# Optimization experiments

Measured on AMD Instinct MI355X. Metric: run time of the kernel, lower is better.

## Reference

```python
import jax, jax.numpy as jnp
import numpy as np
from jax import lax

T = 32
TAU = 2.0
ALPHA = 2.0
V_TH = 1.0
V_RESET = 0.0
MAX_ACTION = 1.0
HID = 750

# ATan surrogate spike function (spikingjelly surrogate.ATan with alpha=2.0)
@jax.custom_vjp
def atan_spike(x):
    return (x >= 0.0).astype(x.dtype)

def _spike_fwd(x):
    return atan_spike(x), x

def _spike_bwd(x, g):
    # d/dx [1/pi * atan(pi/2 * alpha * x) + 1/2] = (alpha/2) / (1 + (pi/2*alpha*x)^2)
    return (g * (ALPHA / 2.0) / (1.0 + (jnp.pi / 2.0 * ALPHA * x) ** 2),)

atan_spike.defvjp(_spike_fwd, _spike_bwd)


def lif_seq(x_seq):
    """MultiStepLIFNode with decay_input=True, hard reset. x_seq: [T,B,D] -> spikes [T,B,D]."""
    def step(v, x):
        h = v + (x - (v - V_RESET)) / TAU  # neuronal_charge
        s = atan_spike(h - V_TH)           # neuronal_fire
        v_new = h * (1.0 - s) + V_RESET * s  # hard reset
        return v_new, s
    v0 = jnp.zeros_like(x_seq[0])
    _, spikes = lax.scan(step, v0, x_seq)
    return spikes


def seq_linear(x_seq, W, b):
    # x_seq: [T,B,I], W: [O,I], b: [O]
    return jnp.einsum('tbi,oi->tbo', x_seq, W) + b


def nonspiking_out(x_seq):
    # NonSpikingLIFNode.forward receives the whole [T,B,D] seq (override bypasses the step loop):
    # v starts at 0 scalar -> v = 0 + (x - (0 - v_reset))/tau = x/tau (v_reset=0), shape [T,B,D]
    return (x_seq + V_RESET) / TAU - 0.0 + 0.0 if False else x_seq / TAU


def setup_inputs() -> dict:
    key = jax.random.key(0)
    ks = jax.random.split(key, 20)
    B, SD, AD, LD = 2048, 256, 64, 128
    def lin(kw, kb, o, i):
        bound = 1.0 / np.sqrt(i)
        W = jax.random.uniform(kw, (o, i), jnp.float32, -bound, bound)
        b = jax.random.uniform(kb, (o,), jnp.float32, -bound, bound)
        return W, b
    W1, b1 = lin(ks[0], ks[1], HID, SD + AD)
    W2, b2 = lin(ks[2], ks[3], HID, HID)
    Wm, bm = lin(ks[4], ks[5], LD, HID)
    Wls, bls = lin(ks[6], ks[7], LD, HID)
    Wd1, bd1 = lin(ks[8], ks[9], HID, SD + LD)
    Wd2, bd2 = lin(ks[10], ks[11], HID, HID)
    Wd3, bd3 = lin(ks[12], ks[13], AD, HID)
    return {
        'state': jax.random.normal(ks[14], (B, SD), jnp.float32),
        'action': jax.random.normal(ks[15], (B, AD), jnp.float32),
        'eps': jax.random.normal(ks[16], (B, LD), jnp.float32),
        'W1': W1, 'b1': b1, 'W2': W2, 'b2': b2,
        'Wm': Wm, 'bm': bm, 'Wls': Wls, 'bls': bls,
        'Wd1': Wd1, 'bd1': bd1, 'Wd2': Wd2, 'bd2': bd2, 'Wd3': Wd3, 'bd3': bd3,
    }


def reference(state, action, eps, W1, b1, W2, b2, Wm, bm, Wls, bls, Wd1, bd1, Wd2, bd2, Wd3, bd3):
    B = state.shape[0]
    # Encoder
    x = jnp.concatenate([state, action], axis=1)            # [B, SD+AD]
    x_seq = jnp.broadcast_to(x, (T,) + x.shape)             # repeat(T,1,1)
    z = lif_seq(seq_linear(x_seq, W1, b1))                  # e1
    z = lif_seq(seq_linear(z, W2, b2))                      # e2
    mean = jnp.max(seq_linear(z, Wm, bm) / TAU, axis=0)     # NonSpiking v = x/tau, then max over T
    log_std = jnp.max(seq_linear(z, Wls, bls) / TAU, axis=0)
    log_std = jnp.clip(log_std, -4.0, 15.0)
    std = jnp.exp(log_std)
    zlat = mean + std * eps
    # Decoder
    d_in = jnp.concatenate([state, zlat], axis=1)
    d_seq = jnp.broadcast_to(d_in, (T,) + d_in.shape)
    a = lif_seq(seq_linear(d_seq, Wd1, bd1))
    a = lif_seq(seq_linear(a, Wd2, bd2))
    a = jnp.max(seq_linear(a, Wd3, bd3) / TAU, axis=0)
    u = MAX_ACTION * jnp.tanh(a)
    return (u, mean, std)
```

## Files before the change

### kernel.cpp

```cpp
#include <hip/hip_runtime.h>
#include <math.h>

#define TT   32
#define NB   2048
#define SDIM 256
#define ADIM 64
#define LDIM 128
#define HID  750
#define KP   768
#define KW   24
#define EIN  320
#define DIN  384
#define NSTEP 12

typedef float    f32x4 __attribute__((ext_vector_type(4)));
typedef int      i32x4 __attribute__((ext_vector_type(4)));
typedef unsigned u32x4 __attribute__((ext_vector_type(4)));

__device__ __forceinline__ f32x4 mfma16(u32x4 a, u32x4 b, f32x4 c) {
    asm("v_mfma_f32_16x16x32_bf16 %0, %1, %2, %0" : "+v"(c) : "v"(a), "v"(b));
    return c;
}
__device__ __forceinline__ i32x4 mfma_i8(u32x4 a, u32x4 b, i32x4 c) {
    asm("v_mfma_i32_16x16x64_i8 %0, %1, %2, %0" : "+v"(c) : "v"(a), "v"(b));
    return c;
}

__device__ __forceinline__ void gload_lds16(void* lds, const void* g) {
    __builtin_amdgcn_global_load_lds(
        (const __attribute__((address_space(1))) unsigned int*)g,
        (__attribute__((address_space(3))) unsigned int*)lds, 16, 0, 0);
}

__device__ __forceinline__ void bfsplit(float v, unsigned& hb, unsigned& lb) {
    unsigned u = __float_as_uint(v);
    hb = (u + 0x7FFFu + ((u >> 16) & 1u)) >> 16;
    float res = v - __uint_as_float(hb << 16);
    unsigned u2 = __float_as_uint(res);
    lb = (u2 + 0x7FFFu + ((u2 >> 16) & 1u)) >> 16;
}

#define I8_E1 589824
#define I8_E2 1179648
#define I8_E3 1277952
#define I8_E4 1376256
#define I8_E5 1425408
__global__ void wsplit_i8_all(const float* __restrict__ W2,
                              const float* __restrict__ Wd2,
                              const float* __restrict__ Wm,
                              const float* __restrict__ Wls,
                              const float* __restrict__ Wd3,
                              char* __restrict__ W2h,  char* __restrict__ W2l,
                              char* __restrict__ Wd2h, char* __restrict__ Wd2l,
                              char* __restrict__ WmlsH, char* __restrict__ WmlsL,
                              char* __restrict__ Wu3h, char* __restrict__ Wu3l) {
    int i = blockIdx.x * blockDim.x + threadIdx.x;
    if (i >= I8_E5) return;
    const float* src; char* dh; char* dl; int rvalid, o_base;
    if (i < I8_E1)      { src = W2;  dh = W2h;  dl = W2l;  rvalid = HID;  o_base = 0; }
    else if (i < I8_E2) { i -= I8_E1; src = Wd2; dh = Wd2h; dl = Wd2l; rvalid = HID;  o_base = 0; }
    else if (i < I8_E3) { i -= I8_E2; src = Wm;  dh = WmlsH; dl = WmlsL; rvalid = LDIM; o_base = 0; }
    else if (i < I8_E4) { i -= I8_E3; src = Wls; dh = WmlsH; dl = WmlsL; rvalid = LDIM; o_base = 128; }
    else                { i -= I8_E4; src = Wd3; dh = Wu3h; dl = Wu3l; rvalid = ADIM; o_base = 0; }
    int r = i / KP, k = i % KP;
    float v = (r < rvalid && k < HID) ? src[r * HID + k] : 0.f;
    int q = (int)rintf(v * 524288.f);
    int lo = (q << 24) >> 24;
    int hi = (q - lo) >> 8;
    int o = o_base + r;
    size_t di = (size_t)((o >> 6) * NSTEP + (k >> 6)) * 4096
              + ((k >> 4) & 3) * 1024 + (o & 63) * 16 + (k & 15);
    dh[di] = (char)hi;
    dl[di] = (char)lo;
}

#define BF_E1 245760
#define BF_E2 540672
__global__ void wsplit_bf_all(const float* __restrict__ W1,
                              const float* __restrict__ Wd1,
                              unsigned short* __restrict__ W1h,
                              unsigned short* __restrict__ W1l,
                              unsigned short* __restrict__ Wd1h,
                              unsigned short* __restrict__ Wd1l) {
    int i = blockIdx.x * blockDim.x + threadIdx.x;
    if (i >= BF_E2) return;
    const float* src; unsigned short* dh; unsigned short* dl; int K, KS;
    if (i < BF_E1) { src = W1; dh = W1h; dl = W1l; K = EIN; KS = 5; }
    else { i -= BF_E1; src = Wd1; dh = Wd1h; dl = Wd1l; K = DIN; KS = 6; }
    int r = i / K, k = i % K;
    float v = (r < HID) ? src[r * K + k] : 0.f;
    unsigned hb, lb;
    bfsplit(v, hb, lb);
    size_t di = ((size_t)((r >> 6) * KS + (k >> 6)) * 8
               + ((k >> 5) & 1) * 4 + ((k >> 3) & 3)) * 512 + (r & 63) * 8 + (k & 7);
    dh[di] = (unsigned short)hb;
    dl[di] = (unsigned short)lb;
}

__global__ void concat_xsplit_enc(const float* __restrict__ state,
                                  const float* __restrict__ action,
                                  unsigned short* __restrict__ Xh,
                                  unsigned short* __restrict__ Xl) {
    int t = blockIdx.x * blockDim.x + threadIdx.x;
    if (t >= NB * (EIN / 8)) return;
    int b = t & (NB - 1), c8 = t >> 11;
    float vals[8];
    if (c8 < SDIM / 8) {
        const float* src = state + (size_t)b * SDIM + c8 * 8;
#pragma unroll
        for (int j = 0; j < 8; ++j) vals[j] = src[j];
    } else {
        const float* src = action + (size_t)b * ADIM + (c8 * 8 - SDIM);
#pragma unroll
        for (int j = 0; j < 8; ++j) vals[j] = src[j];
    }
    unsigned hs[8], ls[8];
#pragma unroll
    for (int j = 0; j < 8; ++j) bfsplit(vals[j], hs[j], ls[j]);
    u32x4 ph, pl;
#pragma unroll
    for (int j = 0; j < 4; ++j) {
        ph[j] = hs[2 * j] | (hs[2 * j + 1] << 16);
        pl[j] = ls[2 * j] | (ls[2 * j + 1] << 16);
    }
    *(u32x4*)(Xh + (size_t)t * 8) = ph;
    *(u32x4*)(Xl + (size_t)t * 8) = pl;
}

__global__ void latent_xsplit(const float* __restrict__ mean_ws,
                              const float* __restrict__ ls_ws,
                              const float* __restrict__ eps,
                              const float* __restrict__ state,
                              float* __restrict__ out,
                              unsigned short* __restrict__ Xh,
                              unsigned short* __restrict__ Xl) {
    int t = blockIdx.x * blockDim.x + threadIdx.x;
    if (t >= NB * (DIN / 8)) return;
    int b = t & (NB - 1), c8 = t >> 11;
    float vals[8];
    if (c8 < SDIM / 8) {
        const float* src = state + (size_t)b * SDIM + c8 * 8;
#pragma unroll
        for (int j = 0; j < 8; ++j) vals[j] = src[j];
    } else {
        int o0 = c8 * 8 - SDIM;
#pragma unroll
        for (int j = 0; j < 8; ++j) {
            int o = o0 + j;
            float m = mean_ws[(size_t)b * LDIM + o];
            float l = ls_ws[(size_t)b * LDIM + o];
            l = fminf(fmaxf(l, -4.0f), 15.0f);
            float s = expf(l);
            vals[j] = m + s * eps[(size_t)b * LDIM + o];
            out[NB * ADIM + (size_t)b * LDIM + o] = m;
            out[NB * ADIM + NB * LDIM + (size_t)b * LDIM + o] = s;
        }
    }
    unsigned hs[8], ls[8];
#pragma unroll
    for (int j = 0; j < 8; ++j) bfsplit(vals[j], hs[j], ls[j]);
    u32x4 ph, pl;
#pragma unroll
    for (int j = 0; j < 4; ++j) {
        ph[j] = hs[2 * j] | (hs[2 * j + 1] << 16);
        pl[j] = ls[2 * j] | (ls[2 * j + 1] << 16);
    }
    *(u32x4*)(Xh + (size_t)t * 8) = ph;
    *(u32x4*)(Xl + (size_t)t * 8) = pl;
}

template<int KS>
__global__ __launch_bounds__(256)
void lif1(const unsigned short* __restrict__ Ah,
          const unsigned short* __restrict__ Al,
          const unsigned short* __restrict__ Wh,
          const unsigned short* __restrict__ Wl,
          const float* __restrict__ bias,
          unsigned* __restrict__ obitsT) {
    __shared__ __align__(16) char smraw[32768];
    const int tid = threadIdx.x, wave = tid >> 6, l = tid & 63;
    const int kg = l >> 4, li = l & 15;
    const int nb = blockIdx.x, n0 = nb * 64, mb = blockIdx.y;
    const int r0 = mb * 128 + wave * 32;
    f32x4 acc[2][4] = {};

    auto stage = [&](int buf, int step) {
        const char* sH = (const char*)(Wh + (size_t)(nb * KS + step) * 4096);
        const char* sL = (const char*)(Wl + (size_t)(nb * KS + step) * 4096);
        char* d = smraw + buf * 16384;
#pragma unroll
        for (int j = 0; j < 2; ++j) {
            gload_lds16(d + j * 4096 + tid * 16, sH + j * 4096 + tid * 16);
            gload_lds16(d + 8192 + j * 4096 + tid * 16, sL + j * 4096 + tid * 16);
        }
    };

    stage(0, 0);
    for (int step = 0; step < KS; ++step) {
        asm volatile("s_waitcnt vmcnt(0)" ::: "memory");
        __builtin_amdgcn_s_barrier();
        __builtin_amdgcn_sched_barrier(0);
        u32x4 ah[2][2], al2[2][2];
#pragma unroll
        for (int kc = 0; kc < 2; ++kc)
#pragma unroll
            for (int mt = 0; mt < 2; ++mt) {
                int r = r0 + mt * 16 + li;
                size_t aoff = ((size_t)(step * 8 + kc * 4 + kg) * NB + r) * 8;
                ah[kc][mt]  = *(const u32x4*)(Ah + aoff);
                al2[kc][mt] = *(const u32x4*)(Al + aoff);
            }
        if (step + 1 < KS) stage((step + 1) & 1, step + 1);
        const char* bufB = smraw + (step & 1) * 16384;
        __builtin_amdgcn_s_setprio(1);
#pragma unroll
        for (int kc = 0; kc < 2; ++kc) {
#pragma unroll
            for (int nt = 0; nt < 4; ++nt) {
                int boff = (kc * 4 + kg) * 1024 + (nt * 16 + li) * 16;
                u32x4 bh = *(const u32x4*)(bufB + boff);
                u32x4 bl = *(const u32x4*)(bufB + 8192 + boff);
#pragma unroll
                for (int mt = 0; mt < 2; ++mt) {
                    acc[mt][nt] = mfma16(ah[kc][mt], bh, acc[mt][nt]);
                    acc[mt][nt] = mfma16(ah[kc][mt], bl, acc[mt][nt]);
                    acc[mt][nt] = mfma16(al2[kc][mt], bh, acc[mt][nt]);
                }
            }
        }
        __builtin_amdgcn_s_setprio(0);
    }
    __syncthreads();

    unsigned* Sb = (unsigned*)smraw;
#pragma unroll
    for (int nt = 0; nt < 4; ++nt) {
        int o = n0 + nt * 16 + li;
        float bo = (o < HID) ? bias[o] : 0.f;
#pragma unroll
        for (int mt = 0; mt < 2; ++mt)
#pragma unroll
            for (int r = 0; r < 4; ++r) {
                float c = acc[mt][nt][r] + bo;
                float v = 0.f;
                unsigned sb = 0u;
#pragma unroll
                for (int t = 0; t < TT; ++t) {
                    float h = 0.5f * (v + c);
                    if (h >= 1.0f) { sb |= (1u << t); v = 0.f; }
                    else           { v = h; }
                }
                Sb[(wave * 32 + mt * 16 + kg * 4 + r) * 64 + nt * 16 + li] = sb;
            }
    }
    __syncthreads();

    for (int rr = 0; rr < 32; ++rr) {
        int row = wave * 32 + rr;
        unsigned wv = Sb[row * 64 + l];
        unsigned myw = 0;
#pragma unroll
        for (int t = 0; t < TT; ++t) {
            unsigned long long m = __ballot((wv >> t) & 1u);
            if ((l & 31) == t) myw = (l < 32) ? (unsigned)m : (unsigned)(m >> 32);
        }
        int b = mb * 128 + row;
        obitsT[((size_t)b * KW + nb * 2 + (l >= 32)) * TT + (l & 31)] = myw;
    }
}

template<int EPI>
__global__ __launch_bounds__(256)
void bitgemm(const unsigned* __restrict__ bitsT,
             const char* __restrict__ Wh,
             const char* __restrict__ Wl,
             const float* __restrict__ bias,
             const float* __restrict__ bias2,
             unsigned* __restrict__ obitsT,
             float* __restrict__ o0,
             float* __restrict__ o1) {
    __shared__ __align__(16) char smraw[32768];
    const int tid = threadIdx.x;
    const int w = tid >> 6, l = tid & 63;
    const int kg = l >> 4, li = l & 15;
    const int nb = blockIdx.x, n0 = nb * 64;
    const int by = blockIdx.y;
    const int b = by * 4 + w;
    const unsigned fld = (kg & 1) * 16;

    i32x4 acc[2][4][2] = {};

    auto stage = [&](int s) {
        char* d = smraw + (s & 3) * 8192;
        const char* sH = Wh + (size_t)(nb * NSTEP + s) * 4096;
        const char* sL = Wl + (size_t)(nb * NSTEP + s) * 4096;
        gload_lds16(d + tid * 16, sH + tid * 16);
        gload_lds16(d + 4096 + tid * 16, sL + tid * 16);
    };
    auto loadA = [&](int s, unsigned (&aw)[2]) {
#pragma unroll
        for (int mt = 0; mt < 2; ++mt)
            aw[mt] = bitsT[((size_t)b * KW + s * 2 + (kg >> 1)) * TT + mt * 16 + li];
    };
    auto compute = [&](int s, const unsigned (&aw)[2]) {
        const char* bufB = smraw + (s & 3) * 8192;
        u32x4 afrag[2];
#pragma unroll
        for (int mt = 0; mt < 2; ++mt) {
            unsigned wv = aw[mt] >> fld;
            u32x4 a;
#pragma unroll
            for (int j = 0; j < 4; ++j)
                a[j] = __umul24((wv >> (4 * j)) & 0xFu, 0x00204081u) & 0x01010101u;
            afrag[mt] = a;
        }
        __builtin_amdgcn_s_setprio(1);
#pragma unroll
        for (int nt = 0; nt < 4; ++nt) {
            int boff = kg * 1024 + (nt * 16 + li) * 16;
            u32x4 bh = *(const u32x4*)(bufB + boff);
            u32x4 bl = *(const u32x4*)(bufB + 4096 + boff);
#pragma unroll
            for (int mt = 0; mt < 2; ++mt) {
                acc[mt][nt][0] = mfma_i8(afrag[mt], bh, acc[mt][nt][0]);
                acc[mt][nt][1] = mfma_i8(afrag[mt], bl, acc[mt][nt][1]);
            }
        }
        __builtin_amdgcn_s_setprio(0);
    };

    unsigned aw[2], awn[2];
    stage(0);
    asm volatile("s_waitcnt vmcnt(0)" ::: "memory");
    __builtin_amdgcn_s_barrier();
    stage(1);
    loadA(0, aw);

    for (int s = 0; s < NSTEP; ++s) {
        asm volatile("s_waitcnt vmcnt(4)" ::: "memory");
        __builtin_amdgcn_s_barrier();
        __builtin_amdgcn_sched_barrier(0);
        if (s + 2 < NSTEP) stage(s + 2);
        if (s + 1 < NSTEP) loadA(s + 1, awn);
        compute(s, aw);
        aw[0] = awn[0];
        aw[1] = awn[1];
    }
    __syncthreads();

    float* Sf = (float*)smraw;
#pragma unroll
    for (int p = 0; p < 2; ++p) {
#pragma unroll
        for (int mt = 0; mt < 2; ++mt)
#pragma unroll
            for (int ntl = 0; ntl < 2; ++ntl) {
                int nt = p * 2 + ntl;
#pragma unroll
                for (int r = 0; r < 4; ++r) {
                    int cmb = (acc[mt][nt][0][r] << 8) + acc[mt][nt][1][r];
                    Sf[(w * 32 + mt * 16 + kg * 4 + r) * 34 + ntl * 16 + li]
                        = (float)cmb * (1.f / 524288.f);
                }
            }
        __syncthreads();

        if (l < 32) {
            int c = l;
            int o = n0 + p * 32 + c;
            if (EPI == 0) {
                float bo = (o < HID) ? bias[o] : 0.f;
                float v = 0.f;
                unsigned sb = 0u;
#pragma unroll
                for (int t = 0; t < TT; ++t) {
                    float h = 0.5f * (v + Sf[(w * 32 + t) * 34 + c] + bo);
                    if (h >= 1.0f) { sb |= (1u << t); v = 0.f; }
                    else           { v = h; }
                }
                if (o >= HID) sb = 0u;
                unsigned myw = 0;
#pragma unroll
                for (int t = 0; t < TT; ++t) {
                    unsigned long long m = __ballot((sb >> t) & 1u);
                    if (l == t) myw = (unsigned)m;
                }
                obitsT[((size_t)b * KW + nb * 2 + p) * TT + l] = myw;
            } else {
                float mx = -1e30f;
#pragma unroll
                for (int t = 0; t < TT; ++t)
                    mx = fmaxf(mx, Sf[(w * 32 + t) * 34 + c]);
                if (EPI == 1) {
                    float bo = (o < LDIM) ? bias[o] : bias2[o - LDIM];
                    float val = 0.5f * (mx + bo);
                    if (o < LDIM) o0[(size_t)b * LDIM + o] = val;
                    else          o1[(size_t)b * LDIM + (o - LDIM)] = val;
                } else {
                    o0[(size_t)b * ADIM + o] = tanhf(0.5f * (mx + bias[o]));
                }
            }
        }
        __syncthreads();
    }
}

extern "C" void kernel_launch(void* const* d_in, const int* in_sizes, int n_in,
                              void* d_out, int out_size, void* d_ws, size_t ws_size,
                              hipStream_t stream) {
    const float* state  = (const float*)d_in[0];
    const float* action = (const float*)d_in[1];
    const float* eps    = (const float*)d_in[2];
    const float* W1  = (const float*)d_in[3];
    const float* b1  = (const float*)d_in[4];
    const float* W2  = (const float*)d_in[5];
    const float* b2  = (const float*)d_in[6];
    const float* Wm  = (const float*)d_in[7];
    const float* bm  = (const float*)d_in[8];
    const float* Wls = (const float*)d_in[9];
    const float* bls = (const float*)d_in[10];
    const float* Wd1 = (const float*)d_in[11];
    const float* bd1 = (const float*)d_in[12];
    const float* Wd2 = (const float*)d_in[13];
    const float* bd2 = (const float*)d_in[14];
    const float* Wd3 = (const float*)d_in[15];
    const float* bd3 = (const float*)d_in[16];
    float* out = (float*)d_out;

    char* ws = (char*)d_ws;
    size_t off = 0;
    auto alloc = [&](size_t bytes) {
        void* p = ws + off;
        off += (bytes + 255) & ~(size_t)255;
        return p;
    };
    unsigned*       bitsT_a = (unsigned*)alloc((size_t)NB * TT * KW * 4);
    unsigned*       bitsT_b = (unsigned*)alloc((size_t)NB * TT * KW * 4);
    float*          mean_ws = (float*)   alloc((size_t)NB * LDIM * 4);
    float*          ls_ws   = (float*)   alloc((size_t)NB * LDIM * 4);
    unsigned short* Xh      = (unsigned short*)alloc((size_t)NB * DIN * 2);
    unsigned short* Xl      = (unsigned short*)alloc((size_t)NB * DIN * 2);
    char*           W2h     = (char*)alloc((size_t)KP * KP);
    char*           W2l     = (char*)alloc((size_t)KP * KP);
    char*           Wd2h    = (char*)alloc((size_t)KP * KP);
    char*           Wd2l    = (char*)alloc((size_t)KP * KP);
    char*           WmlsH   = (char*)alloc((size_t)256 * KP);
    char*           WmlsL   = (char*)alloc((size_t)256 * KP);
    char*           Wu3h    = (char*)alloc((size_t)64 * KP);
    char*           Wu3l    = (char*)alloc((size_t)64 * KP);
    unsigned short* W1h     = (unsigned short*)alloc((size_t)KP * EIN * 2);
    unsigned short* W1l     = (unsigned short*)alloc((size_t)KP * EIN * 2);
    unsigned short* Wd1h    = (unsigned short*)alloc((size_t)KP * DIN * 2);
    unsigned short* Wd1l    = (unsigned short*)alloc((size_t)KP * DIN * 2);

    dim3 blk(256);

    wsplit_i8_all<<<(I8_E5 + 255) / 256, blk, 0, stream>>>(
        W2, Wd2, Wm, Wls, Wd3, W2h, W2l, Wd2h, Wd2l, WmlsH, WmlsL, Wu3h, Wu3l);
    wsplit_bf_all<<<(BF_E2 + 255) / 256, blk, 0, stream>>>(
        W1, Wd1, W1h, W1l, Wd1h, Wd1l);

    concat_xsplit_enc<<<(NB * (EIN / 8) + 255) / 256, blk, 0, stream>>>(state, action, Xh, Xl);
    lif1<5><<<dim3(12, 16), blk, 0, stream>>>(Xh, Xl, W1h, W1l, b1, bitsT_a);
    bitgemm<0><<<dim3(12, NB / 4), blk, 0, stream>>>(bitsT_a, W2h, W2l, b2, nullptr,
                                                     bitsT_b, nullptr, nullptr);
    bitgemm<1><<<dim3(4, NB / 4), blk, 0, stream>>>(bitsT_b, WmlsH, WmlsL, bm, bls,
                                                    nullptr, mean_ws, ls_ws);
    latent_xsplit<<<(NB * (DIN / 8) + 255) / 256, blk, 0, stream>>>(
        mean_ws, ls_ws, eps, state, out, Xh, Xl);

    lif1<6><<<dim3(12, 16), blk, 0, stream>>>(Xh, Xl, Wd1h, Wd1l, bd1, bitsT_a);
    bitgemm<0><<<dim3(12, NB / 4), blk, 0, stream>>>(bitsT_a, Wd2h, Wd2l, bd2, nullptr,
                                                     bitsT_b, nullptr, nullptr);
    bitgemm<2><<<dim3(1, NB / 4), blk, 0, stream>>>(bitsT_b, Wu3h, Wu3l, bd3, nullptr,
                                                    nullptr, out, nullptr);
}
```

Before: 269.1 us.

## Halve lif1 row tile for more blocks; per-wave bitgemm epilogue without block barriers

lif1 now gives each wave 16 rows instead of 32, so each block covers 64 rows and the grid doubles to 12x32 blocks. The intent is better occupancy and a smaller register footprint, at the cost of reloading the staged weight tiles twice as often. The bitgemm epilogue now gives each wave its own padded shared-memory region and processes all 64 columns in one pass with all lanes active. This removes the two-phase loop and the block-wide barriers inside it, and drops the barrier between the LIF and transpose stages in lif1, since those stages now only touch wave-private shared memory. Shared memory in bitgemm grows slightly to fit the per-wave staging.

```diff
diff --git a/kernel.cpp b/kernel.cpp
--- a/kernel.cpp
+++ b/kernel.cpp
@@ -178,11 +178,11 @@
           const float* __restrict__ bias,
           unsigned* __restrict__ obitsT) {
     __shared__ __align__(16) char smraw[32768];
-    const int tid = threadIdx.x, wave = tid >> 6, l = tid & 63;
+    const int tid = threadIdx.x, w = tid >> 6, l = tid & 63;
     const int kg = l >> 4, li = l & 15;
     const int nb = blockIdx.x, n0 = nb * 64, mb = blockIdx.y;
-    const int r0 = mb * 128 + wave * 32;
-    f32x4 acc[2][4] = {};
+    const int r0 = mb * 64 + w * 16;
+    f32x4 acc[4] = {};
 
     auto stage = [&](int buf, int step) {
         const char* sH = (const char*)(Wh + (size_t)(nb * KS + step) * 4096);
@@ -200,16 +200,13 @@
         asm volatile("s_waitcnt vmcnt(0)" ::: "memory");
         __builtin_amdgcn_s_barrier();
         __builtin_amdgcn_sched_barrier(0);
-        u32x4 ah[2][2], al2[2][2];
-#pragma unroll
-        for (int kc = 0; kc < 2; ++kc)
-#pragma unroll
-            for (int mt = 0; mt < 2; ++mt) {
-                int r = r0 + mt * 16 + li;
-                size_t aoff = ((size_t)(step * 8 + kc * 4 + kg) * NB + r) * 8;
-                ah[kc][mt]  = *(const u32x4*)(Ah + aoff);
-                al2[kc][mt] = *(const u32x4*)(Al + aoff);
-            }
+        u32x4 ah[2], al2[2];
+#pragma unroll
+        for (int kc = 0; kc < 2; ++kc) {
+            size_t aoff = ((size_t)(step * 8 + kc * 4 + kg) * NB + r0 + li) * 8;
+            ah[kc]  = *(const u32x4*)(Ah + aoff);
+            al2[kc] = *(const u32x4*)(Al + aoff);
+        }
         if (step + 1 < KS) stage((step + 1) & 1, step + 1);
         const char* bufB = smraw + (step & 1) * 16384;
         __builtin_amdgcn_s_setprio(1);
@@ -220,12 +217,9 @@
                 int boff = (kc * 4 + kg) * 1024 + (nt * 16 + li) * 16;
                 u32x4 bh = *(const u32x4*)(bufB + boff);
                 u32x4 bl = *(const u32x4*)(bufB + 8192 + boff);
-#pragma unroll
-                for (int mt = 0; mt < 2; ++mt) {
-                    acc[mt][nt] = mfma16(ah[kc][mt], bh, acc[mt][nt]);
-                    acc[mt][nt] = mfma16(ah[kc][mt], bl, acc[mt][nt]);
-                    acc[mt][nt] = mfma16(al2[kc][mt], bh, acc[mt][nt]);
-                }
+                acc[nt] = mfma16(ah[kc], bh, acc[nt]);
+                acc[nt] = mfma16(ah[kc], bl, acc[nt]);
+                acc[nt] = mfma16(al2[kc], bh, acc[nt]);
             }
         }
         __builtin_amdgcn_s_setprio(0);
@@ -238,25 +232,22 @@
         int o = n0 + nt * 16 + li;
         float bo = (o < HID) ? bias[o] : 0.f;
 #pragma unroll
-        for (int mt = 0; mt < 2; ++mt)
-#pragma unroll
-            for (int r = 0; r < 4; ++r) {
-                float c = acc[mt][nt][r] + bo;
-                float v = 0.f;
-                unsigned sb = 0u;
-#pragma unroll
-                for (int t = 0; t < TT; ++t) {
-                    float h = 0.5f * (v + c);
-                    if (h >= 1.0f) { sb |= (1u << t); v = 0.f; }
-                    else           { v = h; }
-                }
-                Sb[(wave * 32 + mt * 16 + kg * 4 + r) * 64 + nt * 16 + li] = sb;
+        for (int r = 0; r < 4; ++r) {
+            float c = acc[nt][r] + bo;
+            float v = 0.f;
+            unsigned sb = 0u;
+#pragma unroll
+            for (int t = 0; t < TT; ++t) {
+                float h = 0.5f * (v + c);
+                if (h >= 1.0f) { sb |= (1u << t); v = 0.f; }
+                else           { v = h; }
             }
-    }
-    __syncthreads();
-
-    for (int rr = 0; rr < 32; ++rr) {
-        int row = wave * 32 + rr;
+            Sb[(w * 16 + kg * 4 + r) * 64 + nt * 16 + li] = sb;
+        }
+    }
+
+    for (int rr = 0; rr < 16; ++rr) {
+        int row = w * 16 + rr;
         unsigned wv = Sb[row * 64 + l];
         unsigned myw = 0;
 #pragma unroll
@@ -264,7 +255,7 @@
             unsigned long long m = __ballot((wv >> t) & 1u);
             if ((l & 31) == t) myw = (l < 32) ? (unsigned)m : (unsigned)(m >> 32);
         }
-        int b = mb * 128 + row;
+        int b = mb * 64 + row;
         obitsT[((size_t)b * KW + nb * 2 + (l >= 32)) * TT + (l & 31)] = myw;
     }
 }
@@ -279,7 +270,7 @@
              unsigned* __restrict__ obitsT,
              float* __restrict__ o0,
              float* __restrict__ o1) {
-    __shared__ __align__(16) char smraw[32768];
+    __shared__ __align__(16) char smraw[34816];
     const int tid = threadIdx.x;
     const int w = tid >> 6, l = tid & 63;
     const int kg = l >> 4, li = l & 15;
@@ -348,60 +339,50 @@
     }
     __syncthreads();
 
-    float* Sf = (float*)smraw;
-#pragma unroll
-    for (int p = 0; p < 2; ++p) {
-#pragma unroll
-        for (int mt = 0; mt < 2; ++mt)
-#pragma unroll
-            for (int ntl = 0; ntl < 2; ++ntl) {
-                int nt = p * 2 + ntl;
-#pragma unroll
-                for (int r = 0; r < 4; ++r) {
-                    int cmb = (acc[mt][nt][0][r] << 8) + acc[mt][nt][1][r];
-                    Sf[(w * 32 + mt * 16 + kg * 4 + r) * 34 + ntl * 16 + li]
-                        = (float)cmb * (1.f / 524288.f);
-                }
+    float* Sf = (float*)smraw + (size_t)w * 32 * 66;
+#pragma unroll
+    for (int mt = 0; mt < 2; ++mt)
+#pragma unroll
+        for (int nt = 0; nt < 4; ++nt)
+#pragma unroll
+            for (int r = 0; r < 4; ++r) {
+                int cmb = (acc[mt][nt][0][r] << 8) + acc[mt][nt][1][r];
+                Sf[(mt * 16 + kg * 4 + r) * 66 + nt * 16 + li]
+                    = (float)cmb * (1.f / 524288.f);
             }
-        __syncthreads();
-
-        if (l < 32) {
-            int c = l;
-            int o = n0 + p * 32 + c;
-            if (EPI == 0) {
-                float bo = (o < HID) ? bias[o] : 0.f;
-                float v = 0.f;
-                unsigned sb = 0u;
-#pragma unroll
-                for (int t = 0; t < TT; ++t) {
-                    float h = 0.5f * (v + Sf[(w * 32 + t) * 34 + c] + bo);
-                    if (h >= 1.0f) { sb |= (1u << t); v = 0.f; }
-                    else           { v = h; }
-                }
-                if (o >= HID) sb = 0u;
-                unsigned myw = 0;
-#pragma unroll
-                for (int t = 0; t < TT; ++t) {
-                    unsigned long long m = __ballot((sb >> t) & 1u);
-                    if (l == t) myw = (unsigned)m;
-                }
-                obitsT[((size_t)b * KW + nb * 2 + p) * TT + l] = myw;
-            } else {
-                float mx = -1e30f;
-#pragma unroll
-                for (int t = 0; t < TT; ++t)
-                    mx = fmaxf(mx, Sf[(w * 32 + t) * 34 + c]);
-                if (EPI == 1) {
-                    float bo = (o < LDIM) ? bias[o] : bias2[o - LDIM];
-                    float val = 0.5f * (mx + bo);
-                    if (o < LDIM) o0[(size_t)b * LDIM + o] = val;
-                    else          o1[(size_t)b * LDIM + (o - LDIM)] = val;
-                } else {
-                    o0[(size_t)b * ADIM + o] = tanhf(0.5f * (mx + bias[o]));
-                }
-            }
-        }
-        __syncthreads();
+
+    int o = n0 + l;
+    if (EPI == 0) {
+        float bo = (o < HID) ? bias[o] : 0.f;
+        float v = 0.f;
+        unsigned sb = 0u;
+#pragma unroll
+        for (int t = 0; t < TT; ++t) {
+            float h = 0.5f * (v + Sf[t * 66 + l] + bo);
+            if (h >= 1.0f) { sb |= (1u << t); v = 0.f; }
+            else           { v = h; }
+        }
+        if (o >= HID) sb = 0u;
+        unsigned myw = 0;
+#pragma unroll
+        for (int t = 0; t < TT; ++t) {
+            unsigned long long m = __ballot((sb >> t) & 1u);
+            if ((l & 31) == t) myw = (l < 32) ? (unsigned)m : (unsigned)(m >> 32);
+        }
+        obitsT[((size_t)b * KW + nb * 2 + (l >= 32)) * TT + (l & 31)] = myw;
+    } else {
+        float mx = -1e30f;
+#pragma unroll
+        for (int t = 0; t < TT; ++t)
+            mx = fmaxf(mx, Sf[t * 66 + l]);
+        if (EPI == 1) {
+            float bo = (o < LDIM) ? bias[o] : bias2[o - LDIM];
+            float val = 0.5f * (mx + bo);
+            if (o < LDIM) o0[(size_t)b * LDIM + o] = val;
+            else          o1[(size_t)b * LDIM + (o - LDIM)] = val;
+        } else {
+            o0[(size_t)b * ADIM + l] = tanhf(0.5f * (mx + bias[l]));
+        }
     }
 }
 
@@ -461,7 +442,7 @@
         W1, Wd1, W1h, W1l, Wd1h, Wd1l);
 
     concat_xsplit_enc<<<(NB * (EIN / 8) + 255) / 256, blk, 0, stream>>>(state, action, Xh, Xl);
-    lif1<5><<<dim3(12, 16), blk, 0, stream>>>(Xh, Xl, W1h, W1l, b1, bitsT_a);
+    lif1<5><<<dim3(12, 32), blk, 0, stream>>>(Xh, Xl, W1h, W1l, b1, bitsT_a);
     bitgemm<0><<<dim3(12, NB / 4), blk, 0, stream>>>(bitsT_a, W2h, W2l, b2, nullptr,
                                                      bitsT_b, nullptr, nullptr);
     bitgemm<1><<<dim3(4, NB / 4), blk, 0, stream>>>(bitsT_b, WmlsH, WmlsL, bm, bls,
@@ -469,7 +450,7 @@
     latent_xsplit<<<(NB * (DIN / 8) + 255) / 256, blk, 0, stream>>>(
         mean_ws, ls_ws, eps, state, out, Xh, Xl);
 
-    lif1<6><<<dim3(12, 16), blk, 0, stream>>>(Xh, Xl, Wd1h, Wd1l, bd1, bitsT_a);
+    lif1<6><<<dim3(12, 32), blk, 0, stream>>>(Xh, Xl, Wd1h, Wd1l, bd1, bitsT_a);
     bitgemm<0><<<dim3(12, NB / 4), blk, 0, stream>>>(bitsT_a, Wd2h, Wd2l, bd2, nullptr,
                                                      bitsT_b, nullptr, nullptr);
     bitgemm<2><<<dim3(1, NB / 4), blk, 0, stream>>>(bitsT_b, Wu3h, Wu3l, bd3, nullptr,
```

Result: faster. 224.8 us (-16.4%).
